# Performance work log

Hardware: AMD Instinct MI355X
Metric: run time of the kernel (lower is better)

The kernel has to match this reference:

```python
import jax, jax.numpy as jnp
import numpy as np
from jax import lax

EPS = 1e-8  # pix_norm epsilon (PGGAN convention)


def _conv2d_valid(x, w, b):
    # x: [B,H,W,Cin], w: [kh,kw,Cin,Cout] -> relu(conv) valid padding
    y = lax.conv_general_dilated(x, w, window_strides=(1, 1), padding='VALID',
                                 dimension_numbers=('NHWC', 'HWIO', 'NHWC'))
    return jax.nn.relu(y + b)


def _parametric_depthwise(x, filters):
    # x: [B,H,W,C], filters: [B,kh,kw,C] -> per-sample depthwise conv, SAME, stride 1
    C = x.shape[-1]

    def one(xb, fb):
        # xb: [H,W,C], fb: [kh,kw,C]; depthwise kernel HWIO with I=1, groups=C
        y = lax.conv_general_dilated(xb[None], fb[:, :, None, :], window_strides=(1, 1),
                                     padding='SAME',
                                     dimension_numbers=('NHWC', 'HWIO', 'NHWC'),
                                     feature_group_count=C)
        return y[0]

    return jax.vmap(one)(x, filters)


def setup_inputs() -> dict:
    key = jax.random.key(0)
    ks = jax.random.split(key, 10)
    B, H, W, C = 16, 512, 512, 4
    P, E, F = 8, 128, 4
    s = lambda k, shape, fan: jax.random.normal(k, shape, jnp.float32) * (1.0 / np.sqrt(fan))
    return {
        'input_noise': jax.random.normal(ks[0], (B, H, W, C), jnp.float32),
        'input_params': jax.random.normal(ks[1], (B, P), jnp.float32),
        'W_emb': s(ks[2], (P, E), P),          # Dense(128)
        'b_emb': jnp.zeros((E,), jnp.float32),
        'KT': s(ks[3], (3, 3, E, F), E),        # Conv2DTranspose kernel (acts on 1x1 input)
        'bT': jnp.zeros((F,), jnp.float32),
        'W1': s(ks[4], (9, 9, C, F), 9 * 9 * C),  # gen-init-conv
        'b1': jnp.zeros((F,), jnp.float32),
        'W2': s(ks[5], (9, 9, F, F), 9 * 9 * F),  # gen-init-conv2
        'b2': jnp.zeros((F,), jnp.float32),
    }


def reference(input_noise, input_params, W_emb, b_emb, KT, bT, W1, b1, W2, b2):
    # Dense(128, swish)
    emb = jax.nn.silu(input_params @ W_emb + b_emb)  # [B,128]
    # Reshape to [B,1,1,128] + Conv2DTranspose(k=3, s=3, same): each output pixel (i,j)
    # of the 3x3 grid is input * KT[i,j]; swish activation.
    filters = jax.nn.silu(jnp.einsum('bc,ijcf->bijf', emb, KT) + bT)  # [B,3,3,4]
    # Conv2D(4, 9x9, valid, relu)
    y = _conv2d_valid(input_noise, W1, b1)  # [B,H-8,W-8,4]
    # per-sample dynamic depthwise conv (SAME)
    y = _parametric_depthwise(y, filters)
    # Conv2D(4, 9x9, valid, relu)
    y = _conv2d_valid(y, W2, b2)  # [B,H-16,W-16,4]
    # pix_norm: channelwise RMS normalization
    y = y * lax.rsqrt(jnp.mean(jnp.square(y), axis=-1, keepdims=True) + EPS)
    return y
```

## Files before the change

kernel.cpp:

```cpp
#include <hip/hip_runtime.h>


typedef _Float16 f16;
typedef _Float16 f16x2 __attribute__((ext_vector_type(2)));
typedef _Float16 f16x4 __attribute__((ext_vector_type(4)));
typedef _Float16 f16x8 __attribute__((ext_vector_type(8)));
typedef float f32x4 __attribute__((ext_vector_type(4)));

static __device__ __forceinline__ f32x4 mfma16(f16x8 a, f16x8 b, f32x4 c) {
    return __builtin_amdgcn_mfma_f32_16x16x32_f16(a, b, c, 0, 0, 0);
}

static __device__ __forceinline__ float silu_f(float x) {
    return x / (1.0f + expf(-x));
}

static __device__ __forceinline__ f16x2 split_f(float x) {
    f16x2 r;
    r[0] = (f16)x;
    r[1] = (f16)(x - (float)r[0]);
    return r;
}

#define ACC_STEP(ACC, DY)                                                     \
    do {                                                                      \
        (ACC) = mfma16(ah0, Bh[DY][0], (ACC));                                \
        (ACC) = mfma16(ah1, Bh[DY][1], (ACC));                                \
        (ACC) = mfma16(ah0, Bl[DY][0], (ACC));                                \
        (ACC) = mfma16(ah1, Bl[DY][1], (ACC));                                \
        (ACC) = mfma16(al0, Bh[DY][0], (ACC));                                \
        (ACC) = mfma16(al1, Bh[DY][1], (ACC));                                \
    } while (0)

__global__ __launch_bounds__(256) void k_prep(
    const float* __restrict__ params, const float* __restrict__ W_emb,
    const float* __restrict__ b_emb, const float* __restrict__ KT,
    const float* __restrict__ bT, const float* __restrict__ W1,
    const float* __restrict__ W2,
    f16x8* __restrict__ fragW1, f16x8* __restrict__ fragW2)
{
    __shared__ float s_emb[128];
    __shared__ float s_filt[36];
    __shared__ float s_wc[1936];
    const int t = threadIdx.x, b = blockIdx.x;

    if (t < 128) {
        float sv = b_emb[t];
#pragma unroll
        for (int p = 0; p < 8; ++p)
            sv = fmaf(params[b * 8 + p], W_emb[p * 128 + t], sv);
        s_emb[t] = silu_f(sv);
    }
    __syncthreads();
    if (t < 36) {
        const int ij = t >> 2, ff = t & 3;
        float sv = bT[ff];
        for (int c = 0; c < 128; ++c)
            sv = fmaf(s_emb[c], KT[(ij * 128 + c) * 4 + ff], sv);
        s_filt[t] = silu_f(sv);
    }
    __syncthreads();

    for (int i = t; i < 1936; i += 256) {
        const int f = i & 3, c = (i >> 2) & 3;
        const int dxy = i >> 4, dx = dxy % 11, dy = dxy / 11;
        float sv = 0.f;
#pragma unroll
        for (int i2 = 0; i2 < 3; ++i2)
#pragma unroll
            for (int j2 = 0; j2 < 3; ++j2) {
                const int a = dy - i2, bb = dx - j2;
                if (a >= 0 && a < 9 && bb >= 0 && bb < 9)
                    sv = fmaf(s_filt[(i2 * 3 + j2) * 4 + c],
                              W2[((a * 9 + bb) * 4 + c) * 4 + f], sv);
            }
        s_wc[i] = sv;
    }
    __syncthreads();

    for (int fi = t; fi < 11 * 256; fi += 256) {
        const int dy = fi >> 8, rem = fi & 255;
        const int st = (rem >> 7) & 1, hl = (rem >> 6) & 1, lane = rem & 63;
        const int g = lane >> 4, n = lane & 15, s = n >> 2, f = n & 3;
        f16x8 v;
#pragma unroll
        for (int j = 0; j < 8; ++j) {
            const int k = st * 32 + g * 8 + j;
            const int e = k >> 2, c = k & 3, dx = e - s;
            const float wv = (dx >= 0 && dx < 11)
                ? s_wc[((dy * 11 + dx) * 4 + c) * 4 + f] : 0.f;
            const f16x2 hlv = split_f(wv);
            v[j] = hl ? hlv[1] : hlv[0];
        }
        fragW2[((size_t)b * 11 + dy) * 256 + rem] = v;
    }

    if (b == 0) {
        for (int fi = t; fi < 9 * 256; fi += 256) {
            const int dy = fi >> 8, rem = fi & 255;
            const int st = (rem >> 7) & 1, hl = (rem >> 6) & 1, lane = rem & 63;
            const int g = lane >> 4, n = lane & 15, s = n >> 2, f = n & 3;
            f16x8 v;
#pragma unroll
            for (int j = 0; j < 8; ++j) {
                const int k = st * 32 + g * 8 + j;
                const int e = k >> 2, c = k & 3, dx = e - s;
                const float wv = (dx >= 0 && dx < 9)
                    ? W1[((dy * 9 + dx) * 4 + c) * 4 + f] : 0.f;
                const f16x2 hlv = split_f(wv);
                v[j] = hl ? hlv[1] : hlv[0];
            }
            fragW1[(size_t)dy * 256 + rem] = v;
        }
    }
}

__global__ __launch_bounds__(256, 2) void k_conv1(
    const float* __restrict__ in, const float* __restrict__ b1,
    const f16x8* __restrict__ fragW1, f16* __restrict__ y1)
{
    __shared__ f16x4 s_hi[40][76];
    __shared__ f16x4 s_lo[40][76];
    const int t = threadIdx.x;
    const int x0 = blockIdx.x * 64, y0 = blockIdx.y * 32, b = blockIdx.z;

    const float4* inp = (const float4*)in + (size_t)b * (512 * 512);
    for (int i = t; i < 40 * 76; i += 256) {
        const int rr = i / 76, cc = i % 76;
        const int gy = y0 + rr, gx = x0 + cc;
        float4 v = make_float4(0.f, 0.f, 0.f, 0.f);
        if (gy < 512 && gx < 512) v = inp[gy * 512 + gx];
        f16x4 h, l;
        const f16x2 p0 = split_f(v.x), p1 = split_f(v.y);
        const f16x2 p2 = split_f(v.z), p3 = split_f(v.w);
        h[0] = p0[0]; l[0] = p0[1]; h[1] = p1[0]; l[1] = p1[1];
        h[2] = p2[0]; l[2] = p2[1]; h[3] = p3[0]; l[3] = p3[1];
        s_hi[rr][cc] = h; s_lo[rr][cc] = l;
    }

    const int lane = t & 63, w = t >> 6;
    const int g = lane >> 4, n = lane & 15, s = n >> 2, f = n & 3;

    f16x8 Bh[9][2], Bl[9][2];
#pragma unroll
    for (int dy = 0; dy < 9; ++dy)
#pragma unroll
        for (int st = 0; st < 2; ++st) {
            Bh[dy][st] = fragW1[dy * 256 + st * 128 + lane];
            Bl[dy][st] = fragW1[dy * 256 + st * 128 + 64 + lane];
        }

    __syncthreads();

    const float bias = b1[f];
    f32x4 acc[8];
#pragma unroll
    for (int r = 0; r < 8; ++r) acc[r] = (f32x4){bias, bias, bias, bias};

    const int ai = 4 * (lane & 15) + 2 * g;
#pragma unroll
    for (int ir = 0; ir < 16; ++ir) {
        const f16x4* rh = &s_hi[w * 8 + ir][0];
        const f16x4* rl = &s_lo[w * 8 + ir][0];
        const f16x8 ah0 = *(const f16x8*)(rh + ai);
        const f16x8 ah1 = *(const f16x8*)(rh + ai + 8);
        const f16x8 al0 = *(const f16x8*)(rl + ai);
        const f16x8 al1 = *(const f16x8*)(rl + ai + 8);
#pragma unroll
        for (int r = 0; r < 8; ++r) {
            const int dy = ir - r;
            if (dy >= 0 && dy < 9) ACC_STEP(acc[r], dy);
        }
    }

    const int xb = x0 + 16 * g + s;
#pragma unroll
    for (int r = 0; r < 8; ++r) {
        const int yr = y0 + w * 8 + r;
        if (yr >= 504) continue;
        const size_t rowbase = ((size_t)(b * 504 + yr) * 504) * 8 + f * 2;
#pragma unroll
        for (int q = 0; q < 4; ++q) {
            const int x = xb + 4 * q;
            if (x < 504) {
                const float v = fmaxf(acc[r][q], 0.f);
                *(f16x2*)(y1 + rowbase + (size_t)x * 8) = split_f(v);
            }
        }
    }
}

__global__ __launch_bounds__(256, 2) void k_dwconv2(
    const f16* __restrict__ y1, const float* __restrict__ b2,
    const f16x8* __restrict__ fragW2, float* __restrict__ out)
{
    __shared__ f16x4 s_hi[42][76];
    __shared__ f16x4 s_lo[42][76];
    const int t = threadIdx.x;
    const int x0 = blockIdx.x * 64, y0 = blockIdx.y * 32, b = blockIdx.z;

    for (int i = t; i < 42 * 76; i += 256) {
        const int rr = i / 76, cc = i % 76;
        const int gy = y0 - 1 + rr, gx = x0 - 1 + cc;
        f16x4 h, l;
        if (gy >= 0 && gy < 504 && gx >= 0 && gx < 504) {
            const f16x8 p = *(const f16x8*)(y1 + ((size_t)(b * 504 + gy) * 504 +
                                                  (size_t)gx) * 8);
            h[0] = p[0]; l[0] = p[1]; h[1] = p[2]; l[1] = p[3];
            h[2] = p[4]; l[2] = p[5]; h[3] = p[6]; l[3] = p[7];
        } else {
            h[0] = h[1] = h[2] = h[3] = (f16)0.f;
            l[0] = l[1] = l[2] = l[3] = (f16)0.f;
        }
        s_hi[rr][cc] = h; s_lo[rr][cc] = l;
    }

    const int lane = t & 63, w = t >> 6;
    const int g = lane >> 4, n = lane & 15, s = n >> 2, f = n & 3;

    const f16x8* fr = fragW2 + (size_t)b * 11 * 256;
    f16x8 Bh[11][2], Bl[11][2];
#pragma unroll
    for (int dy = 0; dy < 11; ++dy)
#pragma unroll
        for (int st = 0; st < 2; ++st) {
            Bh[dy][st] = fr[dy * 256 + st * 128 + lane];
            Bl[dy][st] = fr[dy * 256 + st * 128 + 64 + lane];
        }

    __syncthreads();

    const float bias = b2[f];
    f32x4 acc[8];
#pragma unroll
    for (int r = 0; r < 8; ++r) acc[r] = (f32x4){bias, bias, bias, bias};

    const int ai = 4 * (lane & 15) + 2 * g;
#pragma unroll
    for (int ir = 0; ir < 18; ++ir) {
        const f16x4* rh = &s_hi[w * 8 + ir][0];
        const f16x4* rl = &s_lo[w * 8 + ir][0];
        const f16x8 ah0 = *(const f16x8*)(rh + ai);
        const f16x8 ah1 = *(const f16x8*)(rh + ai + 8);
        const f16x8 al0 = *(const f16x8*)(rl + ai);
        const f16x8 al1 = *(const f16x8*)(rl + ai + 8);
#pragma unroll
        for (int r = 0; r < 8; ++r) {
            const int dy = ir - r;
            if (dy >= 0 && dy < 11) ACC_STEP(acc[r], dy);
        }
    }

    const int xb = x0 + 16 * g + s;
#pragma unroll
    for (int r = 0; r < 8; ++r) {
        const int yr = y0 + w * 8 + r;
        const size_t rowbase = ((size_t)((size_t)b * 496 + yr) * 496) * 4 + f;
#pragma unroll
        for (int q = 0; q < 4; ++q) {
            float v = fmaxf(acc[r][q], 0.f);
            float sq = v * v;
            sq += __shfl_xor(sq, 1);
            sq += __shfl_xor(sq, 2);
            const float sc = rsqrtf(sq * 0.25f + 1e-8f);
            const int x = xb + 4 * q;
            if (yr < 496 && x < 496) out[rowbase + (size_t)x * 4] = v * sc;
        }
    }
}

extern "C" void kernel_launch(void* const* d_in, const int* in_sizes, int n_in,
                              void* d_out, int out_size, void* d_ws, size_t ws_size,
                              hipStream_t stream)
{
    const float* noise  = (const float*)d_in[0];
    const float* params = (const float*)d_in[1];
    const float* W_emb  = (const float*)d_in[2];
    const float* b_emb  = (const float*)d_in[3];
    const float* KT     = (const float*)d_in[4];
    const float* bT     = (const float*)d_in[5];
    const float* W1     = (const float*)d_in[6];
    const float* b1     = (const float*)d_in[7];
    const float* W2     = (const float*)d_in[8];
    const float* b2     = (const float*)d_in[9];

    float* out = (float*)d_out;
    f16*   y1  = (f16*)d_ws;
    f16x8* fragW2 = (f16x8*)((char*)d_ws + 65028096);
    f16x8* fragW1 = (f16x8*)((char*)d_ws + 65028096 + 720896);

    k_prep<<<dim3(16), dim3(256), 0, stream>>>(params, W_emb, b_emb, KT, bT,
                                               W1, W2, fragW1, fragW2);

    dim3 grid(8, 16, 16);
    k_conv1<<<grid, dim3(256), 0, stream>>>(noise, b1, fragW1, y1);

    dim3 grid2(8, 16, 16);
    k_dwconv2<<<grid2, dim3(256), 0, stream>>>(y1, b2, fragW2, out);
}
```

Baseline: 149.9 us.

## Reorder conv MFMA loops to stream weights and preload A rows per k-slice

Restructures both 9x9 / 11-row MFMA convolution loops so the outer loop runs over the two k-slices and the filter row, loading the B fragments from global memory inside the loop instead of holding all of them in registers. For each slice it preloads all needed LDS rows into register arrays and then issues the three split-precision MFMAs per output row. This reduces the live weight-fragment register footprint, which may raise occupancy, at the cost of more repeated global/L1 weight loads inside the hot loop.

Result: faster. 142.5 us (-4.9%).

```diff
diff --git a/kernel.cpp b/kernel.cpp
--- a/kernel.cpp
+++ b/kernel.cpp
@@ -21,16 +21,6 @@
     r[1] = (f16)(x - (float)r[0]);
     return r;
 }
-
-#define ACC_STEP(ACC, DY)                                                     \
-    do {                                                                      \
-        (ACC) = mfma16(ah0, Bh[DY][0], (ACC));                                \
-        (ACC) = mfma16(ah1, Bh[DY][1], (ACC));                                \
-        (ACC) = mfma16(ah0, Bl[DY][0], (ACC));                                \
-        (ACC) = mfma16(ah1, Bl[DY][1], (ACC));                                \
-        (ACC) = mfma16(al0, Bh[DY][0], (ACC));                                \
-        (ACC) = mfma16(al1, Bh[DY][1], (ACC));                                \
-    } while (0)
 
 __global__ __launch_bounds__(256) void k_prep(
     const float* __restrict__ params, const float* __restrict__ W_emb,
@@ -141,15 +131,6 @@
     const int lane = t & 63, w = t >> 6;
     const int g = lane >> 4, n = lane & 15, s = n >> 2, f = n & 3;
 
-    f16x8 Bh[9][2], Bl[9][2];
-#pragma unroll
-    for (int dy = 0; dy < 9; ++dy)
-#pragma unroll
-        for (int st = 0; st < 2; ++st) {
-            Bh[dy][st] = fragW1[dy * 256 + st * 128 + lane];
-            Bl[dy][st] = fragW1[dy * 256 + st * 128 + 64 + lane];
-        }
-
     __syncthreads();
 
     const float bias = b1[f];
@@ -159,17 +140,23 @@
 
     const int ai = 4 * (lane & 15) + 2 * g;
 #pragma unroll
-    for (int ir = 0; ir < 16; ++ir) {
-        const f16x4* rh = &s_hi[w * 8 + ir][0];
-        const f16x4* rl = &s_lo[w * 8 + ir][0];
-        const f16x8 ah0 = *(const f16x8*)(rh + ai);
-        const f16x8 ah1 = *(const f16x8*)(rh + ai + 8);
-        const f16x8 al0 = *(const f16x8*)(rl + ai);
-        const f16x8 al1 = *(const f16x8*)(rl + ai + 8);
-#pragma unroll
-        for (int r = 0; r < 8; ++r) {
-            const int dy = ir - r;
-            if (dy >= 0 && dy < 9) ACC_STEP(acc[r], dy);
+    for (int st = 0; st < 2; ++st) {
+        f16x8 Ah[16], Al[16];
+#pragma unroll
+        for (int ir = 0; ir < 16; ++ir) {
+            Ah[ir] = *(const f16x8*)(&s_hi[w * 8 + ir][0] + ai + st * 8);
+            Al[ir] = *(const f16x8*)(&s_lo[w * 8 + ir][0] + ai + st * 8);
+        }
+#pragma unroll
+        for (int dy = 0; dy < 9; ++dy) {
+            const f16x8 Bh = fragW1[dy * 256 + st * 128 + lane];
+            const f16x8 Bl = fragW1[dy * 256 + st * 128 + 64 + lane];
+#pragma unroll
+            for (int r = 0; r < 8; ++r) {
+                acc[r] = mfma16(Ah[r + dy], Bh, acc[r]);
+                acc[r] = mfma16(Ah[r + dy], Bl, acc[r]);
+                acc[r] = mfma16(Al[r + dy], Bh, acc[r]);
+            }
         }
     }
 
@@ -217,16 +204,7 @@
 
     const int lane = t & 63, w = t >> 6;
     const int g = lane >> 4, n = lane & 15, s = n >> 2, f = n & 3;
-
     const f16x8* fr = fragW2 + (size_t)b * 11 * 256;
-    f16x8 Bh[11][2], Bl[11][2];
-#pragma unroll
-    for (int dy = 0; dy < 11; ++dy)
-#pragma unroll
-        for (int st = 0; st < 2; ++st) {
-            Bh[dy][st] = fr[dy * 256 + st * 128 + lane];
-            Bl[dy][st] = fr[dy * 256 + st * 128 + 64 + lane];
-        }
 
     __syncthreads();
 
@@ -237,17 +215,23 @@
 
     const int ai = 4 * (lane & 15) + 2 * g;
 #pragma unroll
-    for (int ir = 0; ir < 18; ++ir) {
-        const f16x4* rh = &s_hi[w * 8 + ir][0];
-        const f16x4* rl = &s_lo[w * 8 + ir][0];
-        const f16x8 ah0 = *(const f16x8*)(rh + ai);
-        const f16x8 ah1 = *(const f16x8*)(rh + ai + 8);
-        const f16x8 al0 = *(const f16x8*)(rl + ai);
-        const f16x8 al1 = *(const f16x8*)(rl + ai + 8);
-#pragma unroll
-        for (int r = 0; r < 8; ++r) {
-            const int dy = ir - r;
-            if (dy >= 0 && dy < 11) ACC_STEP(acc[r], dy);
+    for (int st = 0; st < 2; ++st) {
+        f16x8 Ah[18], Al[18];
+#pragma unroll
+        for (int ir = 0; ir < 18; ++ir) {
+            Ah[ir] = *(const f16x8*)(&s_hi[w * 8 + ir][0] + ai + st * 8);
+            Al[ir] = *(const f16x8*)(&s_lo[w * 8 + ir][0] + ai + st * 8);
+        }
+#pragma unroll
+        for (int dy = 0; dy < 11; ++dy) {
+            const f16x8 Bh = fr[dy * 256 + st * 128 + lane];
+            const f16x8 Bl = fr[dy * 256 + st * 128 + 64 + lane];
+#pragma unroll
+            for (int r = 0; r < 8; ++r) {
+                acc[r] = mfma16(Ah[r + dy], Bh, acc[r]);
+                acc[r] = mfma16(Ah[r + dy], Bl, acc[r]);
+                acc[r] = mfma16(Al[r + dy], Bh, acc[r]);
+            }
         }
     }
 
```
